# Performance work log

Measured on AMD Instinct MI355X. Metric: run time of the kernel, lower is better.

The kernel has to match this reference:

```python
import jax, jax.numpy as jnp
import numpy as np

CHANNELS = 512
SE_CHANNELS = 32


def setup_inputs() -> dict:
    key = jax.random.key(0)
    k_x, k_w1, k_b1, k_w2, k_b2 = jax.random.split(key, 5)
    c, se = CHANNELS, SE_CHANNELS
    x = jax.random.normal(k_x, (256, c, 32, 32), dtype=jnp.float32)
    # torch.nn.Linear default init: U(-1/sqrt(fan_in), 1/sqrt(fan_in))
    s1 = 1.0 / np.sqrt(c)
    s2 = 1.0 / np.sqrt(se)
    fc1_w = jax.random.uniform(k_w1, (se, c), jnp.float32, -s1, s1)
    fc1_b = jax.random.uniform(k_b1, (se,), jnp.float32, -s1, s1)
    fc2_w = jax.random.uniform(k_w2, (2 * c, se), jnp.float32, -s2, s2)
    fc2_b = jax.random.uniform(k_b2, (2 * c,), jnp.float32, -s2, s2)
    return {"x": x, "fc1_w": fc1_w, "fc1_b": fc1_b, "fc2_w": fc2_w, "fc2_b": fc2_b}


def reference(x, fc1_w, fc1_b, fc2_w, fc2_b):
    b, c, h, w = x.shape
    # squeeze: global average pool -> [B, C]
    y = jnp.mean(x, axis=(2, 3))
    # excitation MLP
    y = jax.nn.relu(y @ fc1_w.T + fc1_b)          # [B, se]
    y = y @ fc2_w.T + fc2_b                        # [B, 2C]
    scale, bias = y[:, :c], y[:, c:]
    scale = jax.nn.sigmoid(scale)[:, :, None, None]  # [B, C, 1, 1]
    bias = bias[:, :, None, None]
    return x * scale + bias
```

## Files before the change

### kernel.cpp

```cpp
#include <hip/hip_runtime.h>
#include <math.h>

#define BATCH 256
#define CH 512
#define SE_CH 32
#define HW 1024
#define CHUNK_B 64
#define NCHUNK (BATCH / CHUNK_B)
#define CHUNK_PLANES (CHUNK_B * CH)
#define SUBS 8
#define CPS (CH / SUBS)
#define NA_BLOCKS (CHUNK_B * SUBS)
#define NM_BLOCKS 512

typedef float f32x4 __attribute__((ext_vector_type(4)));

__global__ __launch_bounds__(256) void se_fused(
        const float* __restrict__ x,
        float* __restrict__ out,
        float* __restrict__ mean_ws,
        const float* __restrict__ fc1_w,
        const float* __restrict__ fc1_b,
        const float* __restrict__ fc2_w,
        const float* __restrict__ fc2_b,
        int na, int apply_b0, int mean_p0, int mean_np) {
    const int t = threadIdx.x;
    __shared__ float m[CH];
    __shared__ float se[SE_CH];
    __shared__ float sc[CPS];
    __shared__ float bi[CPS];

    if ((int)blockIdx.x < na) {
        const int ab = blockIdx.x;
        const int b = apply_b0 + (ab >> 3);
        const int sub = ab & 7;

        for (int i = t; i < CH; i += 256)
            m[i] = mean_ws[(size_t)b * CH + i];
        __syncthreads();

        {
            const int o = t >> 3;
            const int p = t & 7;
            const float* wr = fc1_w + o * CH;
            float acc = 0.0f;
#pragma unroll
            for (int j = 0; j < 64; ++j) {
                const int k = p + 8 * j;
                acc = fmaf(wr[k], m[k], acc);
            }
            acc += __shfl_xor(acc, 4, 8);
            acc += __shfl_xor(acc, 2, 8);
            acc += __shfl_xor(acc, 1, 8);
            if (p == 0)
                se[o] = fmaxf(acc + fc1_b[o], 0.0f);
        }
        __syncthreads();

        if (t < 2 * CPS) {
            const int c = sub * CPS + (t & (CPS - 1));
            const int o = (t < CPS) ? c : (CH + c);
            float acc = fc2_b[o];
            const float* wr = fc2_w + o * SE_CH;
#pragma unroll
            for (int k = 0; k < SE_CH; ++k)
                acc = fmaf(wr[k], se[k], acc);
            if (t < CPS)
                sc[t] = 1.0f / (1.0f + expf(-acc));
            else
                bi[t - CPS] = acc;
        }
        __syncthreads();

        const size_t base = ((size_t)b * CH + (size_t)sub * CPS) * HW;
        const f32x4* xp = (const f32x4*)(x + base);
        f32x4* op = (f32x4*)(out + base);
#pragma unroll 4
        for (int p = 0; p < CPS; ++p) {
            const float s = sc[p];
            const float bb = bi[p];
            f32x4 v = xp[p * 256 + t];
            f32x4 r;
            r.x = fmaf(v.x, s, bb);
            r.y = fmaf(v.y, s, bb);
            r.z = fmaf(v.z, s, bb);
            r.w = fmaf(v.w, s, bb);
            __builtin_nontemporal_store(r, &op[p * 256 + t]);
        }
    } else {
        const int lane = t & 63;
        const int wib = t >> 6;
        int wid = ((int)blockIdx.x - na) * 4 + wib;
        const int nw = ((int)gridDim.x - na) * 4;
        for (int p = wid; p < mean_np; p += nw) {
            const f32x4* px = (const f32x4*)(x + (size_t)(mean_p0 + p) * HW);
            float s = 0.0f;
#pragma unroll
            for (int j = 0; j < 4; ++j) {
                f32x4 v = px[lane + j * 64];
                s += (v.x + v.y) + (v.z + v.w);
            }
#pragma unroll
            for (int off = 32; off > 0; off >>= 1)
                s += __shfl_down(s, off, 64);
            if (lane == 0)
                mean_ws[mean_p0 + p] = s * (1.0f / (float)HW);
        }
    }
}

extern "C" void kernel_launch(void* const* d_in, const int* in_sizes, int n_in,
                              void* d_out, int out_size, void* d_ws, size_t ws_size,
                              hipStream_t stream) {
    const float* x     = (const float*)d_in[0];
    const float* fc1_w = (const float*)d_in[1];
    const float* fc1_b = (const float*)d_in[2];
    const float* fc2_w = (const float*)d_in[3];
    const float* fc2_b = (const float*)d_in[4];
    float* out = (float*)d_out;
    float* mean = (float*)d_ws;

    se_fused<<<2048, 256, 0, stream>>>(x, out, mean, fc1_w, fc1_b, fc2_w, fc2_b,
                                       0, 0, 0, CHUNK_PLANES);

    for (int k = 0; k < NCHUNK - 1; ++k) {
        se_fused<<<NA_BLOCKS + NM_BLOCKS, 256, 0, stream>>>(
            x, out, mean, fc1_w, fc1_b, fc2_w, fc2_b,
            NA_BLOCKS, k * CHUNK_B, (k + 1) * CHUNK_PLANES, CHUNK_PLANES);
    }

    se_fused<<<NA_BLOCKS, 256, 0, stream>>>(
        x, out, mean, fc1_w, fc1_b, fc2_w, fc2_b,
        NA_BLOCKS, (NCHUNK - 1) * CHUNK_B, 0, 0);
}
```

Before: 279.7 us.

## Interleave apply and mean blocks, shrink chunks, and reduce two planes per wave

Halves the batch chunk size and splits each batch item into 32 apply sub-blocks, so every pipelined launch has 1024 apply blocks. Apply and mean-reduction blocks now alternate by block index instead of sitting in two contiguous ranges, which spreads both kinds of work evenly across CUs. Each mean wave also reduces two planes at once to raise memory-level parallelism. The cost is twice as many launches and more redundant fc1 computation per apply block, since each block recomputes the full SE hidden layer for only 16 channels.

```diff
diff --git a/kernel.cpp b/kernel.cpp
--- a/kernel.cpp
+++ b/kernel.cpp
@@ -5,13 +5,11 @@
 #define CH 512
 #define SE_CH 32
 #define HW 1024
-#define CHUNK_B 64
+#define CHUNK_B 32
 #define NCHUNK (BATCH / CHUNK_B)
 #define CHUNK_PLANES (CHUNK_B * CH)
-#define SUBS 8
+#define SUBS 32
 #define CPS (CH / SUBS)
-#define NA_BLOCKS (CHUNK_B * SUBS)
-#define NM_BLOCKS 512
 
 typedef float f32x4 __attribute__((ext_vector_type(4)));
 
@@ -25,15 +23,23 @@
         const float* __restrict__ fc2_b,
         int na, int apply_b0, int mean_p0, int mean_np) {
     const int t = threadIdx.x;
-    __shared__ float m[CH];
-    __shared__ float se[SE_CH];
-    __shared__ float sc[CPS];
-    __shared__ float bi[CPS];
+    const int bid = (int)blockIdx.x;
+    const int nm = (int)gridDim.x - na;
 
-    if ((int)blockIdx.x < na) {
-        const int ab = blockIdx.x;
-        const int b = apply_b0 + (ab >> 3);
-        const int sub = ab & 7;
+    bool is_apply;
+    int rid;
+    if (na == 0)            { is_apply = false; rid = bid; }
+    else if (nm == 0)       { is_apply = true;  rid = bid; }
+    else                    { is_apply = !(bid & 1); rid = bid >> 1; }
+
+    if (is_apply) {
+        __shared__ float m[CH];
+        __shared__ float se[SE_CH];
+        __shared__ float sc[CPS];
+        __shared__ float bi[CPS];
+
+        const int b = apply_b0 + (rid >> 5);
+        const int sub = rid & 31;
 
         for (int i = t; i < CH; i += 256)
             m[i] = mean_ws[(size_t)b * CH + i];
@@ -90,21 +96,28 @@
     } else {
         const int lane = t & 63;
         const int wib = t >> 6;
-        int wid = ((int)blockIdx.x - na) * 4 + wib;
-        const int nw = ((int)gridDim.x - na) * 4;
-        for (int p = wid; p < mean_np; p += nw) {
-            const f32x4* px = (const f32x4*)(x + (size_t)(mean_p0 + p) * HW);
-            float s = 0.0f;
+        const int wid = rid * 4 + wib;
+        const int nw = nm * 4;
+        for (int p = wid * 2; p < mean_np; p += nw * 2) {
+            const f32x4* p0 = (const f32x4*)(x + (size_t)(mean_p0 + p) * HW);
+            const f32x4* p1 = (const f32x4*)(x + (size_t)(mean_p0 + p + 1) * HW);
+            float s0 = 0.0f, s1 = 0.0f;
 #pragma unroll
             for (int j = 0; j < 4; ++j) {
-                f32x4 v = px[lane + j * 64];
-                s += (v.x + v.y) + (v.z + v.w);
+                f32x4 v0 = p0[lane + j * 64];
+                f32x4 v1 = p1[lane + j * 64];
+                s0 += (v0.x + v0.y) + (v0.z + v0.w);
+                s1 += (v1.x + v1.y) + (v1.z + v1.w);
             }
 #pragma unroll
-            for (int off = 32; off > 0; off >>= 1)
-                s += __shfl_down(s, off, 64);
-            if (lane == 0)
-                mean_ws[mean_p0 + p] = s * (1.0f / (float)HW);
+            for (int off = 32; off > 0; off >>= 1) {
+                s0 += __shfl_down(s0, off, 64);
+                s1 += __shfl_down(s1, off, 64);
+            }
+            if (lane == 0) {
+                mean_ws[mean_p0 + p]     = s0 * (1.0f / (float)HW);
+                mean_ws[mean_p0 + p + 1] = s1 * (1.0f / (float)HW);
+            }
         }
     }
 }
@@ -124,12 +137,12 @@
                                        0, 0, 0, CHUNK_PLANES);
 
     for (int k = 0; k < NCHUNK - 1; ++k) {
-        se_fused<<<NA_BLOCKS + NM_BLOCKS, 256, 0, stream>>>(
+        se_fused<<<2048, 256, 0, stream>>>(
             x, out, mean, fc1_w, fc1_b, fc2_w, fc2_b,
-            NA_BLOCKS, k * CHUNK_B, (k + 1) * CHUNK_PLANES, CHUNK_PLANES);
+            1024, k * CHUNK_B, (k + 1) * CHUNK_PLANES, CHUNK_PLANES);
     }
 
-    se_fused<<<NA_BLOCKS, 256, 0, stream>>>(
+    se_fused<<<1024, 256, 0, stream>>>(
         x, out, mean, fc1_w, fc1_b, fc2_w, fc2_b,
-        NA_BLOCKS, (NCHUNK - 1) * CHUNK_B, 0, 0);
+        1024, (NCHUNK - 1) * CHUNK_B, 0, 0);
 }
```

New measurement: 311.4 us. +11.3%, slower.

## Shrink pipeline chunks to 16 batches and size apply grid per launch

Applied to the files above, without the earlier changes.

Cuts the batch chunk from 64 to 16, giving 16 launches instead of 4 in the mean/apply software pipeline. Each launch uses 2048 blocks, with a runtime channel-split parameter so the final apply-only launch spreads across many small blocks. Apply loads become nontemporal, so x is not kept in cache on its second read. The aim is a shorter pipeline prologue and epilogue and better occupancy on the tail launch, in exchange for more launch overhead and a per-block MLP recomputed more often.

```diff
diff --git a/kernel.cpp b/kernel.cpp
--- a/kernel.cpp
+++ b/kernel.cpp
@@ -5,13 +5,9 @@
 #define CH 512
 #define SE_CH 32
 #define HW 1024
-#define CHUNK_B 64
+#define CHUNK_B 16
 #define NCHUNK (BATCH / CHUNK_B)
-#define CHUNK_PLANES (CHUNK_B * CH)
-#define SUBS 8
-#define CPS (CH / SUBS)
-#define NA_BLOCKS (CHUNK_B * SUBS)
-#define NM_BLOCKS 512
+#define CP (CHUNK_B * CH)
 
 typedef float f32x4 __attribute__((ext_vector_type(4)));
 
@@ -23,17 +19,20 @@
         const float* __restrict__ fc1_b,
         const float* __restrict__ fc2_w,
         const float* __restrict__ fc2_b,
-        int na, int apply_b0, int mean_p0, int mean_np) {
+        int na, int subs_lg, int apply_b0, int mean_p0, int mean_np) {
     const int t = threadIdx.x;
-    __shared__ float m[CH];
-    __shared__ float se[SE_CH];
-    __shared__ float sc[CPS];
-    __shared__ float bi[CPS];
+    const int bid = (int)blockIdx.x;
 
-    if ((int)blockIdx.x < na) {
-        const int ab = blockIdx.x;
-        const int b = apply_b0 + (ab >> 3);
-        const int sub = ab & 7;
+    if (bid < na) {
+        __shared__ float m[CH];
+        __shared__ float sev[SE_CH];
+        __shared__ float sc[256];
+        __shared__ float bi[256];
+
+        const int subs = 1 << subs_lg;
+        const int cps = CH >> subs_lg;
+        const int b = apply_b0 + (bid >> subs_lg);
+        const int sub = bid & (subs - 1);
 
         for (int i = t; i < CH; i += 256)
             m[i] = mean_ws[(size_t)b * CH + i];
@@ -53,33 +52,33 @@
             acc += __shfl_xor(acc, 2, 8);
             acc += __shfl_xor(acc, 1, 8);
             if (p == 0)
-                se[o] = fmaxf(acc + fc1_b[o], 0.0f);
+                sev[o] = fmaxf(acc + fc1_b[o], 0.0f);
         }
         __syncthreads();
 
-        if (t < 2 * CPS) {
-            const int c = sub * CPS + (t & (CPS - 1));
-            const int o = (t < CPS) ? c : (CH + c);
+        if (t < 2 * cps) {
+            const int cl = t & (cps - 1);
+            const int c = sub * cps + cl;
+            const int o = (t < cps) ? c : (CH + c);
             float acc = fc2_b[o];
             const float* wr = fc2_w + o * SE_CH;
 #pragma unroll
             for (int k = 0; k < SE_CH; ++k)
-                acc = fmaf(wr[k], se[k], acc);
-            if (t < CPS)
-                sc[t] = 1.0f / (1.0f + expf(-acc));
+                acc = fmaf(wr[k], sev[k], acc);
+            if (t < cps)
+                sc[cl] = 1.0f / (1.0f + expf(-acc));
             else
-                bi[t - CPS] = acc;
+                bi[cl] = acc;
         }
         __syncthreads();
 
-        const size_t base = ((size_t)b * CH + (size_t)sub * CPS) * HW;
+        const size_t base = ((size_t)b * CH + (size_t)sub * cps) * HW;
         const f32x4* xp = (const f32x4*)(x + base);
         f32x4* op = (f32x4*)(out + base);
-#pragma unroll 4
-        for (int p = 0; p < CPS; ++p) {
+        for (int p = 0; p < cps; ++p) {
             const float s = sc[p];
             const float bb = bi[p];
-            f32x4 v = xp[p * 256 + t];
+            f32x4 v = __builtin_nontemporal_load(&xp[p * 256 + t]);
             f32x4 r;
             r.x = fmaf(v.x, s, bb);
             r.y = fmaf(v.y, s, bb);
@@ -90,8 +89,9 @@
     } else {
         const int lane = t & 63;
         const int wib = t >> 6;
-        int wid = ((int)blockIdx.x - na) * 4 + wib;
+        const int rid = bid - na;
         const int nw = ((int)gridDim.x - na) * 4;
+        const int wid = rid * 4 + wib;
         for (int p = wid; p < mean_np; p += nw) {
             const f32x4* px = (const f32x4*)(x + (size_t)(mean_p0 + p) * HW);
             float s = 0.0f;
@@ -101,10 +101,10 @@
                 s += (v.x + v.y) + (v.z + v.w);
             }
 #pragma unroll
-            for (int off = 32; off > 0; off >>= 1)
-                s += __shfl_down(s, off, 64);
+            for (int off = 32; off; off >>= 1)
+                s += __shfl_xor(s, off, 64);
             if (lane == 0)
-                mean_ws[mean_p0 + p] = s * (1.0f / (float)HW);
+                mean_ws[mean_p0 + p] = s * (1.0f / 1024.0f);
         }
     }
 }
@@ -121,15 +121,15 @@
     float* mean = (float*)d_ws;
 
     se_fused<<<2048, 256, 0, stream>>>(x, out, mean, fc1_w, fc1_b, fc2_w, fc2_b,
-                                       0, 0, 0, CHUNK_PLANES);
+                                       0, 0, 0, 0, CP);
 
     for (int k = 0; k < NCHUNK - 1; ++k) {
-        se_fused<<<NA_BLOCKS + NM_BLOCKS, 256, 0, stream>>>(
+        se_fused<<<2048, 256, 0, stream>>>(
             x, out, mean, fc1_w, fc1_b, fc2_w, fc2_b,
-            NA_BLOCKS, k * CHUNK_B, (k + 1) * CHUNK_PLANES, CHUNK_PLANES);
+            512, 5, k * CHUNK_B, (k + 1) * CP, CP);
     }
 
-    se_fused<<<NA_BLOCKS, 256, 0, stream>>>(
+    se_fused<<<2048, 256, 0, stream>>>(
         x, out, mean, fc1_w, fc1_b, fc2_w, fc2_b,
-        NA_BLOCKS, (NCHUNK - 1) * CHUNK_B, 0, 0);
+        2048, 7, (NCHUNK - 1) * CHUNK_B, 0, 0);
 }
```

After: 287.1 us. 1.03x slower.
